# Performance work log

Measured on AMD Instinct MI355X. Metric: run time of the kernel, lower is better.

Reference implementation:

```python
import jax, jax.numpy as jnp
import numpy as np

MAX_AGENTS = 64
IN_DIM = 256
HID_DIM = 512
OUT_DIM = 256
MAX_CHILDREN = 8
BATCH = 1024


def setup_inputs() -> dict:
    key = jax.random.key(0)
    k1, k2, k3, k4, k5 = jax.random.split(key, 5)
    W1 = jax.random.normal(k1, (MAX_AGENTS, IN_DIM, HID_DIM), dtype=jnp.float32) * 0.02
    b1 = jnp.zeros((MAX_AGENTS, HID_DIM), dtype=jnp.float32)
    W2 = jax.random.normal(k2, (MAX_AGENTS, HID_DIM, OUT_DIM), dtype=jnp.float32) * 0.02
    b2 = jnp.zeros((MAX_AGENTS, OUT_DIM), dtype=jnp.float32)
    router_weights = jax.random.normal(k3, (MAX_AGENTS, HID_DIM, MAX_CHILDREN), dtype=jnp.float32) * 0.01
    agent_indices = jax.random.randint(k4, (BATCH,), 0, MAX_AGENTS, dtype=jnp.int64 if jax.config.jax_enable_x64 else jnp.int32)
    x = jax.random.normal(k5, (BATCH, IN_DIM), dtype=jnp.float32)
    return {
        "x": x,
        "W1": W1,
        "b1": b1,
        "W2": W2,
        "b2": b2,
        "router_weights": router_weights,
        "agent_indices": agent_indices,
    }


def reference(x, W1, b1, W2, b2, router_weights, agent_indices):
    # Gather per-sample weights (same as torch advanced indexing W1[agent_indices])
    w1 = W1[agent_indices]           # [B, In, Hid]
    b1g = b1[agent_indices]          # [B, Hid]
    w2 = W2[agent_indices]           # [B, Hid, Out]
    b2g = b2[agent_indices]          # [B, Out]
    rw = router_weights[agent_indices]  # [B, Hid, C]

    # per-sample MLP: bmm with a singleton row -> einsum
    h = jax.nn.relu(jnp.einsum('bi,bih->bh', x, w1) + b1g)      # [B, Hid]
    out = jnp.einsum('bh,bho->bo', h, w2) + b2g                 # [B, Out]
    r_logits = jnp.einsum('bh,bhc->bc', h, rw)                  # [B, C]
    return (h, out, r_logits)
```

## Files before the change

kernel.cpp:

```cpp
#include <hip/hip_runtime.h>

#define IN_DIM   256
#define HID_DIM  512
#define OUT_DIM  256
#define N_CHILD  8
#define BATCH    1024

#define SB    16
#define XPAD  20
#define MAXCH 128

extern "C" __global__ __launch_bounds__(1024)
void prep_sort(const int* __restrict__ raw, int* __restrict__ sorted,
               int* __restrict__ ch_agent, int* __restrict__ ch_start,
               int* __restrict__ ch_len)
{
    __shared__ int cnt[64], cnt2[64], start[64];
    __shared__ int is32, totch;
    const int t = threadIdx.x;
    if (t < 64) { cnt[t] = 0; cnt2[t] = 0; }
    if (t == 0) is32 = 0;
    __syncthreads();
    if (raw[2 * (t & 511) + 1] != 0) is32 = 1;
    __syncthreads();
    const int a = (is32 ? raw[t] : raw[2 * t]) & 63;
    atomicAdd(&cnt[a], 1);
    __syncthreads();
    if (t < 64) {
        const int c   = cnt[t];
        const int nch = (c + SB - 1) / SB;
        int sc = c, sn = nch;
        #pragma unroll
        for (int d = 1; d < 64; d <<= 1) {
            const int vc = __shfl_up(sc, d);
            const int vn = __shfl_up(sn, d);
            if (t >= d) { sc += vc; sn += vn; }
        }
        const int off = sc - c;
        start[t] = off;
        const int chb = sn - nch;
        for (int p = 0, j = 0; p < c; p += SB, ++j) {
            ch_agent[chb + j] = t;
            ch_start[chb + j] = off + p;
            ch_len[chb + j]   = (c - p < SB) ? (c - p) : SB;
        }
        if (t == 63) totch = sn;
    }
    __syncthreads();
    if (t >= totch && t < MAXCH) ch_len[t] = 0;
    const int pos = start[a] + atomicAdd(&cnt2[a], 1);
    sorted[pos] = t;
}

extern "C" __global__ __launch_bounds__(256)
void k1_mlp1(const float* __restrict__ x, const float* __restrict__ W1,
             const float* __restrict__ b1, const float* __restrict__ rw,
             const int* __restrict__ sorted, const int* __restrict__ ch_agent,
             const int* __restrict__ ch_start, const int* __restrict__ ch_len,
             float* __restrict__ h_out, float* __restrict__ r_out)
{
    const int chunk = blockIdx.x;
    const int len = ch_len[chunk];
    if (len == 0) return;
    const int a  = ch_agent[chunk];
    const int cs = ch_start[chunk];
    const int t  = threadIdx.x;
    const int bcol = blockIdx.y * 64;

    __shared__ float xT[IN_DIM * XPAD];
    __shared__ float wS[2][64 * 64];
    __shared__ int   sid[SB];

    if (t < SB) sid[t] = sorted[cs + (t < len ? t : len - 1)];
    __syncthreads();

    #pragma unroll
    for (int s = 0; s < SB; ++s)
        xT[t * XPAD + s] = x[(size_t)sid[s] * IN_DIM + t];

    const float* Wb = W1 + (size_t)a * IN_DIM * HID_DIM + bcol;
    #pragma unroll
    for (int i = 0; i < 4; ++i) {
        const int id  = t + i * 256;
        const int row = id >> 4;
        const int c4  = (id & 15) * 4;
        *(float4*)(&wS[0][row * 64 + c4]) =
            *(const float4*)(Wb + (size_t)row * HID_DIM + c4);
    }
    __syncthreads();

    const int cg = t & 15;
    const int kq = (t >> 4) & 3;
    const int w  = t >> 6;
    const bool act = (w * 4) < len;

    float acc[16];
    #pragma unroll
    for (int i = 0; i < 16; ++i) acc[i] = 0.f;

    for (int p = 0; p < IN_DIM / 64; ++p) {
        if (p < 3) {
            const int nb = (p + 1) & 1;
            const float* Wp = Wb + (size_t)(p + 1) * 64 * HID_DIM;
            #pragma unroll
            for (int i = 0; i < 4; ++i) {
                const int id  = t + i * 256;
                const int row = id >> 4;
                const int c4  = (id & 15) * 4;
                *(float4*)(&wS[nb][row * 64 + c4]) =
                    *(const float4*)(Wp + (size_t)row * HID_DIM + c4);
            }
        }
        if (act) {
            const float* wb = wS[p & 1];
            #pragma unroll
            for (int i = 0; i < 16; ++i) {
                const int row = kq * 16 + i;
                const float4 wv = *(const float4*)(&wb[row * 64 + cg * 4]);
                const float4 xv = *(const float4*)(&xT[(p * 64 + row) * XPAD + w * 4]);
                const float wa[4] = {wv.x, wv.y, wv.z, wv.w};
                const float xa[4] = {xv.x, xv.y, xv.z, xv.w};
                #pragma unroll
                for (int c = 0; c < 4; ++c)
                    #pragma unroll
                    for (int s = 0; s < 4; ++s)
                        acc[c * 4 + s] = fmaf(wa[c], xa[s], acc[c * 4 + s]);
            }
        }
        __syncthreads();
    }

    if (!act) return;

    #pragma unroll
    for (int i = 0; i < 16; ++i) {
        acc[i] += __shfl_xor(acc[i], 16);
        acc[i] += __shfl_xor(acc[i], 32);
    }

    const float4 bv = *(const float4*)(b1 + a * HID_DIM + bcol + cg * 4);
    const float ba[4] = {bv.x, bv.y, bv.z, bv.w};
    float hv[16];
    #pragma unroll
    for (int c = 0; c < 4; ++c)
        #pragma unroll
        for (int s = 0; s < 4; ++s)
            hv[c * 4 + s] = fmaxf(acc[c * 4 + s] + ba[c], 0.f);

    if (kq == 0) {
        #pragma unroll
        for (int s = 0; s < 4; ++s) {
            float4 v = make_float4(hv[0 * 4 + s], hv[1 * 4 + s],
                                   hv[2 * 4 + s], hv[3 * 4 + s]);
            *(float4*)(h_out + (size_t)sid[w * 4 + s] * HID_DIM + bcol + cg * 4) = v;
        }
    }

    float rp[32];
    #pragma unroll
    for (int i = 0; i < 32; ++i) rp[i] = 0.f;
    const float* rwa = rw + (size_t)a * HID_DIM * N_CHILD + (size_t)(bcol + cg * 4) * N_CHILD;
    #pragma unroll
    for (int j = 0; j < 4; ++j)
        #pragma unroll
        for (int ch = 0; ch < 8; ++ch) {
            const float rv = rwa[j * N_CHILD + ch];
            #pragma unroll
            for (int s = 0; s < 4; ++s)
                rp[s * 8 + ch] = fmaf(hv[j * 4 + s], rv, rp[s * 8 + ch]);
        }
    #pragma unroll
    for (int i = 0; i < 32; ++i) {
        rp[i] += __shfl_xor(rp[i], 1);
        rp[i] += __shfl_xor(rp[i], 2);
        rp[i] += __shfl_xor(rp[i], 4);
        rp[i] += __shfl_xor(rp[i], 8);
    }
    if (cg == 0 && kq == 0) {
        #pragma unroll
        for (int s = 0; s < 4; ++s) {
            const int sg = w * 4 + s;
            if (sg < len) {
                float* rdst = r_out + (size_t)sid[sg] * N_CHILD;
                #pragma unroll
                for (int ch = 0; ch < 8; ++ch)
                    atomicAdd(rdst + ch, rp[s * 8 + ch]);
            }
        }
    }
}

extern "C" __global__ __launch_bounds__(256)
void k2_mlp2(const float* __restrict__ h, const float* __restrict__ W2,
             const float* __restrict__ b2,
             const int* __restrict__ sorted, const int* __restrict__ ch_agent,
             const int* __restrict__ ch_start, const int* __restrict__ ch_len,
             float* __restrict__ o_out)
{
    const int chunk = blockIdx.x;
    const int len = ch_len[chunk];
    if (len == 0) return;
    const int a  = ch_agent[chunk];
    const int cs = ch_start[chunk];
    const int t  = threadIdx.x;
    const int bcol = blockIdx.y * 64;
    const int kb   = blockIdx.z * 256;

    __shared__ float hT[2][64 * XPAD];
    __shared__ float wS[2][64 * 64];
    __shared__ int   sid[SB];

    if (t < SB) sid[t] = sorted[cs + (t < len ? t : len - 1)];
    __syncthreads();

    const float* Wb = W2 + (size_t)a * HID_DIM * OUT_DIM + bcol;
    {
        const int row = t & 63;
        const int sb  = (t >> 6) * 4;
        #pragma unroll
        for (int j = 0; j < 4; ++j)
            hT[0][row * XPAD + sb + j] =
                h[(size_t)sid[sb + j] * HID_DIM + kb + row];
        #pragma unroll
        for (int i = 0; i < 4; ++i) {
            const int id  = t + i * 256;
            const int r2  = id >> 4;
            const int c4  = (id & 15) * 4;
            *(float4*)(&wS[0][r2 * 64 + c4]) =
                *(const float4*)(Wb + (size_t)(kb + r2) * OUT_DIM + c4);
        }
    }
    __syncthreads();

    const int cg = t & 15;
    const int kq = (t >> 4) & 3;
    const int w  = t >> 6;
    const bool act = (w * 4) < len;

    float acc[16];
    #pragma unroll
    for (int i = 0; i < 16; ++i) acc[i] = 0.f;

    for (int p = 0; p < 4; ++p) {
        if (p < 3) {
            const int nb = (p + 1) & 1;
            const int k0 = kb + (p + 1) * 64;
            const int row = t & 63;
            const int sb  = (t >> 6) * 4;
            #pragma unroll
            for (int j = 0; j < 4; ++j)
                hT[nb][row * XPAD + sb + j] =
                    h[(size_t)sid[sb + j] * HID_DIM + k0 + row];
            const float* Wp = Wb + (size_t)k0 * OUT_DIM;
            #pragma unroll
            for (int i = 0; i < 4; ++i) {
                const int id  = t + i * 256;
                const int r2  = id >> 4;
                const int c4  = (id & 15) * 4;
                *(float4*)(&wS[nb][r2 * 64 + c4]) =
                    *(const float4*)(Wp + (size_t)r2 * OUT_DIM + c4);
            }
        }
        if (act) {
            const float* wb = wS[p & 1];
            const float* hb = hT[p & 1];
            #pragma unroll
            for (int i = 0; i < 16; ++i) {
                const int row = kq * 16 + i;
                const float4 wv = *(const float4*)(&wb[row * 64 + cg * 4]);
                const float4 xv = *(const float4*)(&hb[row * XPAD + w * 4]);
                const float wa[4] = {wv.x, wv.y, wv.z, wv.w};
                const float xa[4] = {xv.x, xv.y, xv.z, xv.w};
                #pragma unroll
                for (int c = 0; c < 4; ++c)
                    #pragma unroll
                    for (int s = 0; s < 4; ++s)
                        acc[c * 4 + s] = fmaf(wa[c], xa[s], acc[c * 4 + s]);
            }
        }
        __syncthreads();
    }

    if (!act) return;
    #pragma unroll
    for (int i = 0; i < 16; ++i) {
        acc[i] += __shfl_xor(acc[i], 16);
        acc[i] += __shfl_xor(acc[i], 32);
    }
    if (kq == 0) {
        float4 bv = make_float4(0.f, 0.f, 0.f, 0.f);
        if (blockIdx.z == 0)
            bv = *(const float4*)(b2 + a * OUT_DIM + bcol + cg * 4);
        #pragma unroll
        for (int s = 0; s < 4; ++s) {
            const int g = w * 4 + s;
            if (g < len) {
                float* op = o_out + (size_t)sid[g] * OUT_DIM + bcol + cg * 4;
                atomicAdd(op + 0, acc[0 * 4 + s] + bv.x);
                atomicAdd(op + 1, acc[1 * 4 + s] + bv.y);
                atomicAdd(op + 2, acc[2 * 4 + s] + bv.z);
                atomicAdd(op + 3, acc[3 * 4 + s] + bv.w);
            }
        }
    }
}

extern "C" void kernel_launch(void* const* d_in, const int* in_sizes, int n_in,
                              void* d_out, int out_size, void* d_ws, size_t ws_size,
                              hipStream_t stream) {
    const float* x  = (const float*)d_in[0];
    const float* W1 = (const float*)d_in[1];
    const float* b1 = (const float*)d_in[2];
    const float* W2 = (const float*)d_in[3];
    const float* b2 = (const float*)d_in[4];
    const float* rw = (const float*)d_in[5];
    const int* raw  = (const int*)d_in[6];

    int* ws       = (int*)d_ws;
    int* sorted   = ws;
    int* ch_agent = ws + 1024;
    int* ch_start = ws + 1152;
    int* ch_len   = ws + 1280;

    float* out   = (float*)d_out;
    float* h_out = out;
    float* o_out = h_out + (size_t)BATCH * HID_DIM;
    float* r_out = o_out + (size_t)BATCH * OUT_DIM;

    hipMemsetAsync(o_out, 0,
                   (size_t)BATCH * (OUT_DIM + N_CHILD) * sizeof(float), stream);
    hipLaunchKernelGGL(prep_sort, dim3(1), dim3(1024), 0, stream,
                       raw, sorted, ch_agent, ch_start, ch_len);
    hipLaunchKernelGGL(k1_mlp1, dim3(MAXCH, 8), dim3(256), 0, stream,
                       x, W1, b1, rw, sorted, ch_agent, ch_start, ch_len,
                       h_out, r_out);
    hipLaunchKernelGGL(k2_mlp2, dim3(MAXCH, 4, 2), dim3(256), 0, stream,
                       h_out, W2, b2, sorted, ch_agent, ch_start, ch_len, o_out);
}
```

Measured before the change: 134.1 us.

## Fold output zeroing into prep kernel and drop double-buffered shared tiles

Removes the separate hipMemsetAsync by giving prep_sort four extra blocks that zero the output and router-logit buffers with float4 stores. Both MLP kernels switch from double-buffered to single-buffered shared-memory weight tiles, with a sync before and after each load. The k-row mapping becomes interleaved (i*4+kq), which changes the LDS access pattern. In k1, threads with kq != 0 now exit right after the reduction. Halving shared memory may allow more resident blocks, but loads no longer overlap compute.

```diff
diff --git a/kernel.cpp b/kernel.cpp
--- a/kernel.cpp
+++ b/kernel.cpp
@@ -13,11 +13,18 @@
 extern "C" __global__ __launch_bounds__(1024)
 void prep_sort(const int* __restrict__ raw, int* __restrict__ sorted,
                int* __restrict__ ch_agent, int* __restrict__ ch_start,
-               int* __restrict__ ch_len)
+               int* __restrict__ ch_len, float* __restrict__ zdst)
 {
+    const int t = threadIdx.x;
+    if (blockIdx.x > 0) {
+        const int total4 = (BATCH * (OUT_DIM + N_CHILD)) / 4;
+        const float4 z = make_float4(0.f, 0.f, 0.f, 0.f);
+        for (int i = (blockIdx.x - 1) * 1024 + t; i < total4; i += 4 * 1024)
+            ((float4*)zdst)[i] = z;
+        return;
+    }
     __shared__ int cnt[64], cnt2[64], start[64];
     __shared__ int is32, totch;
-    const int t = threadIdx.x;
     if (t < 64) { cnt[t] = 0; cnt2[t] = 0; }
     if (t == 0) is32 = 0;
     __syncthreads();
@@ -68,7 +75,7 @@
     const int bcol = blockIdx.y * 64;
 
     __shared__ float xT[IN_DIM * XPAD];
-    __shared__ float wS[2][64 * 64];
+    __shared__ float wS[64 * 64];
     __shared__ int   sid[SB];
 
     if (t < SB) sid[t] = sorted[cs + (t < len ? t : len - 1)];
@@ -79,16 +86,6 @@
         xT[t * XPAD + s] = x[(size_t)sid[s] * IN_DIM + t];
 
     const float* Wb = W1 + (size_t)a * IN_DIM * HID_DIM + bcol;
-    #pragma unroll
-    for (int i = 0; i < 4; ++i) {
-        const int id  = t + i * 256;
-        const int row = id >> 4;
-        const int c4  = (id & 15) * 4;
-        *(float4*)(&wS[0][row * 64 + c4]) =
-            *(const float4*)(Wb + (size_t)row * HID_DIM + c4);
-    }
-    __syncthreads();
-
     const int cg = t & 15;
     const int kq = (t >> 4) & 3;
     const int w  = t >> 6;
@@ -99,24 +96,21 @@
     for (int i = 0; i < 16; ++i) acc[i] = 0.f;
 
     for (int p = 0; p < IN_DIM / 64; ++p) {
-        if (p < 3) {
-            const int nb = (p + 1) & 1;
-            const float* Wp = Wb + (size_t)(p + 1) * 64 * HID_DIM;
-            #pragma unroll
-            for (int i = 0; i < 4; ++i) {
-                const int id  = t + i * 256;
-                const int row = id >> 4;
-                const int c4  = (id & 15) * 4;
-                *(float4*)(&wS[nb][row * 64 + c4]) =
-                    *(const float4*)(Wp + (size_t)row * HID_DIM + c4);
-            }
-        }
+        __syncthreads();
+        #pragma unroll
+        for (int i = 0; i < 4; ++i) {
+            const int id  = t + i * 256;
+            const int row = id >> 4;
+            const int c4  = (id & 15) * 4;
+            *(float4*)(&wS[row * 64 + c4]) =
+                *(const float4*)(Wb + (size_t)(p * 64 + row) * HID_DIM + c4);
+        }
+        __syncthreads();
         if (act) {
-            const float* wb = wS[p & 1];
             #pragma unroll
             for (int i = 0; i < 16; ++i) {
-                const int row = kq * 16 + i;
-                const float4 wv = *(const float4*)(&wb[row * 64 + cg * 4]);
+                const int row = i * 4 + kq;
+                const float4 wv = *(const float4*)(&wS[row * 64 + cg * 4]);
                 const float4 xv = *(const float4*)(&xT[(p * 64 + row) * XPAD + w * 4]);
                 const float wa[4] = {wv.x, wv.y, wv.z, wv.w};
                 const float xa[4] = {xv.x, xv.y, xv.z, xv.w};
@@ -127,7 +121,6 @@
                         acc[c * 4 + s] = fmaf(wa[c], xa[s], acc[c * 4 + s]);
             }
         }
-        __syncthreads();
     }
 
     if (!act) return;
@@ -138,6 +131,8 @@
         acc[i] += __shfl_xor(acc[i], 32);
     }
 
+    if (kq != 0) return;
+
     const float4 bv = *(const float4*)(b1 + a * HID_DIM + bcol + cg * 4);
     const float ba[4] = {bv.x, bv.y, bv.z, bv.w};
     float hv[16];
@@ -147,19 +142,18 @@
         for (int s = 0; s < 4; ++s)
             hv[c * 4 + s] = fmaxf(acc[c * 4 + s] + ba[c], 0.f);
 
-    if (kq == 0) {
-        #pragma unroll
-        for (int s = 0; s < 4; ++s) {
-            float4 v = make_float4(hv[0 * 4 + s], hv[1 * 4 + s],
-                                   hv[2 * 4 + s], hv[3 * 4 + s]);
-            *(float4*)(h_out + (size_t)sid[w * 4 + s] * HID_DIM + bcol + cg * 4) = v;
-        }
+    #pragma unroll
+    for (int s = 0; s < 4; ++s) {
+        float4 v = make_float4(hv[0 * 4 + s], hv[1 * 4 + s],
+                               hv[2 * 4 + s], hv[3 * 4 + s]);
+        *(float4*)(h_out + (size_t)sid[w * 4 + s] * HID_DIM + bcol + cg * 4) = v;
     }
 
     float rp[32];
     #pragma unroll
     for (int i = 0; i < 32; ++i) rp[i] = 0.f;
-    const float* rwa = rw + (size_t)a * HID_DIM * N_CHILD + (size_t)(bcol + cg * 4) * N_CHILD;
+    const float* rwa = rw + (size_t)a * HID_DIM * N_CHILD
+                          + (size_t)(bcol + cg * 4) * N_CHILD;
     #pragma unroll
     for (int j = 0; j < 4; ++j)
         #pragma unroll
@@ -176,7 +170,7 @@
         rp[i] += __shfl_xor(rp[i], 4);
         rp[i] += __shfl_xor(rp[i], 8);
     }
-    if (cg == 0 && kq == 0) {
+    if (cg == 0) {
         #pragma unroll
         for (int s = 0; s < 4; ++s) {
             const int sg = w * 4 + s;
@@ -206,69 +200,49 @@
     const int bcol = blockIdx.y * 64;
     const int kb   = blockIdx.z * 256;
 
-    __shared__ float hT[2][64 * XPAD];
-    __shared__ float wS[2][64 * 64];
+    __shared__ float hT[64 * XPAD];
+    __shared__ float wS[64 * 64];
     __shared__ int   sid[SB];
 
     if (t < SB) sid[t] = sorted[cs + (t < len ? t : len - 1)];
     __syncthreads();
 
     const float* Wb = W2 + (size_t)a * HID_DIM * OUT_DIM + bcol;
-    {
-        const int row = t & 63;
-        const int sb  = (t >> 6) * 4;
-        #pragma unroll
-        for (int j = 0; j < 4; ++j)
-            hT[0][row * XPAD + sb + j] =
-                h[(size_t)sid[sb + j] * HID_DIM + kb + row];
+    const int cg = t & 15;
+    const int kq = (t >> 4) & 3;
+    const int w  = t >> 6;
+    const bool act = (w * 4) < len;
+
+    float acc[16];
+    #pragma unroll
+    for (int i = 0; i < 16; ++i) acc[i] = 0.f;
+
+    for (int p = 0; p < 4; ++p) {
+        const int k0 = kb + p * 64;
+        __syncthreads();
+        {
+            const int row = t & 63;
+            const int sb  = (t >> 6) * 4;
+            #pragma unroll
+            for (int j = 0; j < 4; ++j)
+                hT[row * XPAD + sb + j] =
+                    h[(size_t)sid[sb + j] * HID_DIM + k0 + row];
+        }
         #pragma unroll
         for (int i = 0; i < 4; ++i) {
             const int id  = t + i * 256;
             const int r2  = id >> 4;
             const int c4  = (id & 15) * 4;
-            *(float4*)(&wS[0][r2 * 64 + c4]) =
-                *(const float4*)(Wb + (size_t)(kb + r2) * OUT_DIM + c4);
-        }
-    }
-    __syncthreads();
-
-    const int cg = t & 15;
-    const int kq = (t >> 4) & 3;
-    const int w  = t >> 6;
-    const bool act = (w * 4) < len;
-
-    float acc[16];
-    #pragma unroll
-    for (int i = 0; i < 16; ++i) acc[i] = 0.f;
-
-    for (int p = 0; p < 4; ++p) {
-        if (p < 3) {
-            const int nb = (p + 1) & 1;
-            const int k0 = kb + (p + 1) * 64;
-            const int row = t & 63;
-            const int sb  = (t >> 6) * 4;
-            #pragma unroll
-            for (int j = 0; j < 4; ++j)
-                hT[nb][row * XPAD + sb + j] =
-                    h[(size_t)sid[sb + j] * HID_DIM + k0 + row];
-            const float* Wp = Wb + (size_t)k0 * OUT_DIM;
-            #pragma unroll
-            for (int i = 0; i < 4; ++i) {
-                const int id  = t + i * 256;
-                const int r2  = id >> 4;
-                const int c4  = (id & 15) * 4;
-                *(float4*)(&wS[nb][r2 * 64 + c4]) =
-                    *(const float4*)(Wp + (size_t)r2 * OUT_DIM + c4);
-            }
-        }
+            *(float4*)(&wS[r2 * 64 + c4]) =
+                *(const float4*)(Wb + (size_t)(k0 + r2) * OUT_DIM + c4);
+        }
+        __syncthreads();
         if (act) {
-            const float* wb = wS[p & 1];
-            const float* hb = hT[p & 1];
             #pragma unroll
             for (int i = 0; i < 16; ++i) {
-                const int row = kq * 16 + i;
-                const float4 wv = *(const float4*)(&wb[row * 64 + cg * 4]);
-                const float4 xv = *(const float4*)(&hb[row * XPAD + w * 4]);
+                const int row = i * 4 + kq;
+                const float4 wv = *(const float4*)(&wS[row * 64 + cg * 4]);
+                const float4 xv = *(const float4*)(&hT[row * XPAD + w * 4]);
                 const float wa[4] = {wv.x, wv.y, wv.z, wv.w};
                 const float xa[4] = {xv.x, xv.y, xv.z, xv.w};
                 #pragma unroll
@@ -278,7 +252,6 @@
                         acc[c * 4 + s] = fmaf(wa[c], xa[s], acc[c * 4 + s]);
             }
         }
-        __syncthreads();
     }
 
     if (!act) return;
@@ -327,10 +300,8 @@
     float* o_out = h_out + (size_t)BATCH * HID_DIM;
     float* r_out = o_out + (size_t)BATCH * OUT_DIM;
 
-    hipMemsetAsync(o_out, 0,
-                   (size_t)BATCH * (OUT_DIM + N_CHILD) * sizeof(float), stream);
-    hipLaunchKernelGGL(prep_sort, dim3(1), dim3(1024), 0, stream,
-                       raw, sorted, ch_agent, ch_start, ch_len);
+    hipLaunchKernelGGL(prep_sort, dim3(5), dim3(1024), 0, stream,
+                       raw, sorted, ch_agent, ch_start, ch_len, o_out);
     hipLaunchKernelGGL(k1_mlp1, dim3(MAXCH, 8), dim3(256), 0, stream,
                        x, W1, b1, rw, sorted, ch_agent, ch_start, ch_len,
                        h_out, r_out);
```

Result: no change. 132.6 us (-1.1%).
